# Kernel tuning notes

Measured on AMD Instinct MI355X. Metric: run time of the kernel, lower is better.

The kernel has to match this reference:

```python
import jax, jax.numpy as jnp
import numpy as np

B, S, D, H, T = 128, 256, 256, 1024, 128  # batch, src_len, input/output_dim, hidden, target_len


def setup_inputs() -> dict:
    key = jax.random.key(0)
    ks = jax.random.split(key, 16)
    sc = 0.05

    def p(k, shape):
        return (jax.random.normal(k, shape, jnp.float32) * sc)

    return {
        "x": jax.random.normal(ks[0], (B, S, D), jnp.float32),
        "x_target": jax.random.normal(ks[1], (B, T, D), jnp.float32),
        # encoder bidirectional LSTM (1 layer): gates order i,f,g,o (PyTorch)
        "enc_Wih_f": p(ks[2], (4 * H, D)),  "enc_Whh_f": p(ks[3], (4 * H, H)), "enc_b_f": p(ks[4], (4 * H,)),
        "enc_Wih_b": p(ks[5], (4 * H, D)),  "enc_Whh_b": p(ks[6], (4 * H, H)), "enc_b_b": p(ks[7], (4 * H,)),
        # decoder bidirectional LSTM (1 layer)
        "dec_Wih_f": p(ks[8], (4 * H, D)),  "dec_Whh_f": p(ks[9], (4 * H, H)), "dec_b_f": p(ks[10], (4 * H,)),
        "dec_Wih_b": p(ks[11], (4 * H, D)), "dec_Whh_b": p(ks[12], (4 * H, H)), "dec_b_b": p(ks[13], (4 * H,)),
        # decoder head: Linear(2H -> D)
        "mlp_W": p(ks[14], (D, 2 * H)), "mlp_b": p(ks[15], (D,)),
    }


def lstm_cell(x, h, c, Wih, Whh, b):
    # x: [B, Din], h/c: [B, H]; PyTorch gate order i, f, g, o
    g = x @ Wih.T + h @ Whh.T + b
    i, f, gg, o = jnp.split(g, 4, axis=-1)
    c = jax.nn.sigmoid(f) * c + jax.nn.sigmoid(i) * jnp.tanh(gg)
    h = jax.nn.sigmoid(o) * jnp.tanh(c)
    return h, c


def run_dir(xs, Wih, Whh, b, reverse):
    # xs: [S, B, Din]; returns final (h, c) for one direction (zero init, like torch LSTM without h0)
    h0 = jnp.zeros((xs.shape[1], Whh.shape[1]), xs.dtype)
    c0 = jnp.zeros_like(h0)

    def step(carry, xt):
        h, c = lstm_cell(xt, *carry, Wih, Whh, b)
        return (h, c), None

    (h, c), _ = jax.lax.scan(step, (h0, c0), xs, reverse=reverse)
    return h, c


def reference(x, x_target, enc_Wih_f, enc_Whh_f, enc_b_f, enc_Wih_b, enc_Whh_b, enc_b_b,
              dec_Wih_f, dec_Whh_f, dec_b_f, dec_Wih_b, dec_Whh_b, dec_b_b, mlp_W, mlp_b):
    xs = jnp.transpose(x, (1, 0, 2))  # [S, B, D], time-major
    hf, cf = run_dir(xs, enc_Wih_f, enc_Whh_f, enc_b_f, reverse=False)
    hb, cb = run_dir(xs, enc_Wih_b, enc_Whh_b, enc_b_b, reverse=True)

    dec_in = x[:, -1, :]  # [B, D]

    def step(carry, _):
        hf, cf, hb, cb, inp = carry
        # bidirectional LSTM on a length-1 sequence: both directions see the same step
        hf2, cf2 = lstm_cell(inp, hf, cf, dec_Wih_f, dec_Whh_f, dec_b_f)
        hb2, cb2 = lstm_cell(inp, hb, cb, dec_Wih_b, dec_Whh_b, dec_b_b)
        out = jnp.concatenate([hf2, hb2], axis=-1) @ mlp_W.T + mlp_b  # [B, D]
        # teacher_forcing_ratio = 0.0 -> always feed model output back
        return (hf2, cf2, hb2, cb2, out), out

    _, outs = jax.lax.scan(step, (hf, cf, hb, cb, dec_in), None, length=T)
    return jnp.transpose(outs, (1, 0, 2))  # [B, T, D]
```

## Files before the change

kernel.cpp:

```cpp
#include <hip/hip_runtime.h>
#include <stdint.h>


typedef __attribute__((ext_vector_type(8))) short bfx8;
typedef __attribute__((ext_vector_type(4))) float f32x4;
typedef __attribute__((ext_vector_type(4))) unsigned short u16x4;
typedef unsigned short ushort_t;
typedef unsigned long long u64;

#define NWG 256
#define MFMA(a,b,c) __builtin_amdgcn_mfma_f32_16x16x32_bf16((a),(b),(c),0,0,0)
#define WAITVM(N) { asm volatile("s_waitcnt vmcnt(" #N ")" ::: "memory"); __builtin_amdgcn_sched_barrier(0); }
#define WAITLG(N) { asm volatile("s_waitcnt lgkmcnt(" #N ")" ::: "memory"); __builtin_amdgcn_sched_barrier(0); }
#define SBAR()    { __builtin_amdgcn_s_barrier(); __builtin_amdgcn_sched_barrier(0); }

__device__ __forceinline__ unsigned short f2bf(float f){
  unsigned u = __float_as_uint(f);
  u += 0x7FFFu + ((u >> 16) & 1u);
  return (unsigned short)(u >> 16);
}
__device__ __forceinline__ float bf2f(unsigned short h){
  return __uint_as_float(((unsigned)h) << 16);
}
__device__ __forceinline__ float sigm(float x){ return 1.f/(1.f + __expf(-x)); }
__device__ __forceinline__ float tanh_(float x){ return 1.f - 2.f/(__expf(2.f*x) + 1.f); }

__device__ __forceinline__ void stage16(const void* g, void* l){
  __builtin_amdgcn_global_load_lds((const __attribute__((address_space(1))) void*)g,
                                   (__attribute__((address_space(3))) void*)l,
                                   16, 0, 0);
}
__device__ __forceinline__ void stage16c(const void* g, void* l){
  __builtin_amdgcn_global_load_lds((const __attribute__((address_space(1))) void*)g,
                                   (__attribute__((address_space(3))) void*)l,
                                   16, 0, 0x11);
}

__device__ __forceinline__ bfx8 ld16c(const ushort_t* p){
  const u64* q = (const u64*)p;
  u64 a = __hip_atomic_load(q,     __ATOMIC_RELAXED, __HIP_MEMORY_SCOPE_AGENT);
  u64 b = __hip_atomic_load(q + 1, __ATOMIC_RELAXED, __HIP_MEMORY_SCOPE_AGENT);
  union { u64 u[2]; bfx8 v; } x; x.u[0] = a; x.u[1] = b; return x.v;
}
__device__ __forceinline__ void sth2(ushort_t* p, unsigned short v){
  __hip_atomic_store(p, v, __ATOMIC_RELAXED, __HIP_MEMORY_SCOPE_AGENT);
}

__device__ __forceinline__ void cvt2(const f32x4& a, const f32x4& b, bfx8& hi, bfx8& lo){
#pragma unroll
  for (int j = 0; j < 4; ++j){
    unsigned short h0 = f2bf(a[j]);
    unsigned short h1 = f2bf(b[j]);
    hi[j]   = (short)h0; lo[j]   = (short)f2bf(a[j] - bf2f(h0));
    hi[4+j] = (short)h1; lo[4+j] = (short)f2bf(b[j] - bf2f(h1));
  }
}

__device__ __forceinline__ void bar(unsigned* flags, int nflags, int me, unsigned gen){
  __syncthreads();
  if (threadIdx.x == 0)
    __hip_atomic_store(&flags[me], gen, __ATOMIC_RELAXED, __HIP_MEMORY_SCOPE_AGENT);
  if (threadIdx.x < 64){
    const int l = threadIdx.x;
    for (;;){
      unsigned mn = 0xFFFFFFFFu;
      for (int o = l; o < nflags; o += 64){
        unsigned v = __hip_atomic_load(&flags[o], __ATOMIC_RELAXED, __HIP_MEMORY_SCOPE_AGENT);
        mn = mn < v ? mn : v;
      }
      if (__all((int)(mn >= gen))) break;
      __builtin_amdgcn_s_sleep(1);
    }
  }
  __syncthreads();
}

struct Frags { bfx8 awh0, awh1, awl0, awl1, bh0, bh1, bl0, bl1; };

template<int ENC>
__device__ __forceinline__ void cell_step(
    const float*    __restrict__ Wih,
    const ushort_t* __restrict__ WhH,
    const ushort_t* __restrict__ WhL,
    const float*    __restrict__ bias,
    const float*    __restrict__ xsl,
    const ushort_t* __restrict__ iph,
    const ushort_t* __restrict__ ipl,
    const ushort_t* __restrict__ hh,
    const ushort_t* __restrict__ hl,
    ushort_t* __restrict__ outh, ushort_t* __restrict__ outl,
    float (&creg)[2][2],
    int r0, int n0, int b0, ushort_t* LDS)
{
  const int tid  = threadIdx.x;
  const int lane = tid & 63;
  const int wv   = tid >> 6;
  const int wm   = wv >> 1, wn = wv & 1;
  const int lr   = tid >> 3;
  const int lc   = tid & 7;
  const int cb   = lane >> 4;
  const int fr   = lane & 15;
  const int sc8  = lc ^ (lr & 7);
  const int sx   = fr & 7;
  const int rwa0 = wm*32 + fr, rwa1 = rwa0 + 16;
  const int rwb0 = wn*32 + fr, rwb1 = rwb0 + 16;

  const int ra = r0 + lr, rb = ra + 32;
  const float* wih0 = Wih + (size_t)((ra & 3)*1024 + (ra >> 2))*256 + sc8*8;
  const float* wih1 = Wih + (size_t)((rb & 3)*1024 + (rb >> 2))*256 + sc8*8;
  const float *xs0 = nullptr, *xs1 = nullptr;
  const ushort_t *ih0 = nullptr, *ih1 = nullptr, *il0 = nullptr, *il1 = nullptr;
  if (ENC){
    xs0 = xsl + (size_t)(b0 + lr)*65536 + sc8*8;
    xs1 = xs0 + (size_t)32*65536;
  } else {
    ih0 = iph + (size_t)(b0 + lr)*256 + sc8*8;  ih1 = ih0 + 32*256;
    il0 = ipl + (size_t)(b0 + lr)*256 + sc8*8;  il1 = il0 + 32*256;
  }

  const ushort_t* sb; size_t sstr; int srow0;
  if      (wv == 0){ sb = WhH; sstr = 1024; srow0 = r0; }
  else if (wv == 1){ sb = WhL; sstr = 1024; srow0 = r0; }
  else if (wv == 2){ sb = hh;  sstr = 2048; srow0 = b0; }
  else             { sb = hl;  sstr = 2048; srow0 = b0; }
  const int srw = lane >> 3;
  const int sg  = (lane & 7) ^ srw;
  const ushort_t* pj[8];
#pragma unroll
  for (int j = 0; j < 8; ++j)
    pj[j] = sb + (size_t)(srow0 + j*8 + srw)*sstr + sg*8;
  ushort_t* ldsb[3];
#pragma unroll
  for (int bp = 0; bp < 3; ++bp)
    ldsb[bp] = LDS + 16384 + bp*16384 + wv*4096;

  auto ISSUE = [&](int c, int bp){
    const int ko = (c - 4)*64;
    if (wv < 2){
#pragma unroll
      for (int j = 0; j < 8; ++j)
        stage16(pj[j] + ko, ldsb[bp] + j*512);
    } else {
#pragma unroll
      for (int j = 0; j < 8; ++j)
        stage16c(pj[j] + ko, ldsb[bp] + j*512);
    }
  };

  f32x4 acc[2][2] = {};
  auto rdf = [&](const ushort_t* buf, int ks, Frags& f){
    const int ga = (((ks << 2) + cb) ^ sx) << 3;
    f.awh0 = *(const bfx8*)(buf +         rwa0*64 + ga);
    f.awh1 = *(const bfx8*)(buf +         rwa1*64 + ga);
    f.awl0 = *(const bfx8*)(buf + 4096  + rwa0*64 + ga);
    f.awl1 = *(const bfx8*)(buf + 4096  + rwa1*64 + ga);
    f.bh0  = *(const bfx8*)(buf + 8192  + rwb0*64 + ga);
    f.bh1  = *(const bfx8*)(buf + 8192  + rwb1*64 + ga);
    f.bl0  = *(const bfx8*)(buf + 12288 + rwb0*64 + ga);
    f.bl1  = *(const bfx8*)(buf + 12288 + rwb1*64 + ga);
  };
  auto mm12 = [&](const Frags& f){
    acc[0][0] = MFMA(f.awh0, f.bh0, acc[0][0]);
    acc[0][0] = MFMA(f.awh0, f.bl0, acc[0][0]);
    acc[0][0] = MFMA(f.awl0, f.bh0, acc[0][0]);
    acc[0][1] = MFMA(f.awh0, f.bh1, acc[0][1]);
    acc[0][1] = MFMA(f.awh0, f.bl1, acc[0][1]);
    acc[0][1] = MFMA(f.awl0, f.bh1, acc[0][1]);
    acc[1][0] = MFMA(f.awh1, f.bh0, acc[1][0]);
    acc[1][0] = MFMA(f.awh1, f.bl0, acc[1][0]);
    acc[1][0] = MFMA(f.awl1, f.bh0, acc[1][0]);
    acc[1][1] = MFMA(f.awh1, f.bh1, acc[1][1]);
    acc[1][1] = MFMA(f.awh1, f.bl1, acc[1][1]);
    acc[1][1] = MFMA(f.awl1, f.bh1, acc[1][1]);
  };

  f32x4 rw0a, rw0b, rw1a, rw1b, rxa0, rxb0, rxa1, rxb1;
  bfx8 cwh0, cwh1, cwl0, cwl1, cah0, cah1, cal0, cal1;
  auto LOADRAW = [&](int kc){
    rw0a = *(const f32x4*)(wih0 + kc);  rw0b = *(const f32x4*)(wih0 + kc + 4);
    rw1a = *(const f32x4*)(wih1 + kc);  rw1b = *(const f32x4*)(wih1 + kc + 4);
    if (ENC){
      rxa0 = *(const f32x4*)(xs0 + kc); rxb0 = *(const f32x4*)(xs0 + kc + 4);
      rxa1 = *(const f32x4*)(xs1 + kc); rxb1 = *(const f32x4*)(xs1 + kc + 4);
    } else {
      cah0 = ld16c(ih0 + kc);  cah1 = ld16c(ih1 + kc);
      cal0 = ld16c(il0 + kc);  cal1 = ld16c(il1 + kc);
    }
  };
  auto CVT = [&](){
    cvt2(rw0a, rw0b, cwh0, cwl0);
    cvt2(rw1a, rw1b, cwh1, cwl1);
    if (ENC){ cvt2(rxa0, rxb0, cah0, cal0); cvt2(rxa1, rxb1, cah1, cal1); }
  };

  LOADRAW(0);
  ISSUE(4, 0); ISSUE(5, 1); ISSUE(6, 2);
  CVT();

  for (int c = 0; c < 4; ++c){
    *(bfx8*)(LDS +         lr    *64 + lc*8) = cwh0;
    *(bfx8*)(LDS +        (lr+32)*64 + lc*8) = cwh1;
    *(bfx8*)(LDS + 4096 +  lr    *64 + lc*8) = cwl0;
    *(bfx8*)(LDS + 4096 + (lr+32)*64 + lc*8) = cwl1;
    *(bfx8*)(LDS + 8192 +  lr    *64 + lc*8) = cah0;
    *(bfx8*)(LDS + 8192 + (lr+32)*64 + lc*8) = cah1;
    *(bfx8*)(LDS + 12288 + lr    *64 + lc*8) = cal0;
    *(bfx8*)(LDS + 12288 +(lr+32)*64 + lc*8) = cal1;
    WAITLG(0); SBAR();
    if (c < 3) LOADRAW((c + 1)*64);
    Frags f0, f1;
    rdf(LDS, 0, f0);
    rdf(LDS, 1, f1);
    WAITLG(8);
    mm12(f0);
    WAITLG(0); SBAR();
    if (c < 3) CVT();
    mm12(f1);
  }

  int bi = 0;
  for (int i = 4; i <= 19; ++i){
    if (i < 18)      { WAITVM(16); }
    else if (i == 18){ WAITVM(8); }
    else             { WAITVM(0); }
    SBAR();
    const ushort_t* buf = LDS + 16384 + bi*16384;
    Frags f0, f1;
    rdf(buf, 0, f0);
    rdf(buf, 1, f1);
    WAITLG(8);
    mm12(f0);
    WAITLG(0); SBAR();
    if (i <= 16) ISSUE(i + 3, bi);
    mm12(f1);
    bi = (bi == 2) ? 0 : bi + 1;
  }

#pragma unroll
  for (int m = 0; m < 2; ++m){
    const int n = n0 + wm*8 + m*4 + cb;
    const float bi_ = bias[n];
    const float bf_ = bias[1024 + n];
    const float bg_ = bias[2048 + n];
    const float bo_ = bias[3072 + n];
#pragma unroll
    for (int nb = 0; nb < 2; ++nb){
      const int b = b0 + wn*32 + nb*16 + fr;
      float gi = acc[m][nb][0] + bi_;
      float gf = acc[m][nb][1] + bf_;
      float gg = acc[m][nb][2] + bg_;
      float go = acc[m][nb][3] + bo_;
      float c_new = sigm(gf)*creg[m][nb] + sigm(gi)*tanh_(gg);
      float h_new = sigm(go)*tanh_(c_new);
      creg[m][nb] = c_new;
      unsigned short hi = f2bf(h_new);
      sth2(&outh[(size_t)b*2048 + n], hi);
      sth2(&outl[(size_t)b*2048 + n], f2bf(h_new - bf2f(hi)));
    }
  }
}

__device__ __forceinline__ void mlp_gemm(
    const ushort_t* __restrict__ hch, const ushort_t* __restrict__ hcl,
    const ushort_t* __restrict__ mWh, const ushort_t* __restrict__ mWl,
    float* __restrict__ Part, int wg, ushort_t* LDS)
{
  const int tid = threadIdx.x, lane = tid & 63, wv = tid >> 6;
  const int cb = lane >> 4, fr = lane & 15, sx = fr & 7;
  const int wgl = wg & 127, kh = wg >> 7;
  const int d0 = (wgl >> 3)*16, b0 = (wgl & 7)*16;
  const int kb = kh*1024 + wv*256;
  const int srw = lane >> 3, sg = (lane & 7) ^ srw;

  const ushort_t* ps[4] = { mWh, mWl, hch, hcl };
  const int pr0[4] = { d0, d0, b0, b0 };
  const ushort_t* pj[4][2];
#pragma unroll
  for (int p = 0; p < 4; ++p)
#pragma unroll
    for (int j = 0; j < 2; ++j)
      pj[p][j] = ps[p] + (size_t)(pr0[p] + j*8 + srw)*2048 + kb + sg*8;
  ushort_t* lb[3];
#pragma unroll
  for (int bp = 0; bp < 3; ++bp)
    lb[bp] = LDS + 16384 + (wv*3 + bp)*4096;

  auto ISSUE = [&](int c, int bp){
    const int ko = c*64;
#pragma unroll
    for (int p = 0; p < 4; ++p)
#pragma unroll
      for (int j = 0; j < 2; ++j){
        if (p < 2) stage16 (pj[p][j] + ko, lb[bp] + p*1024 + j*512);
        else       stage16c(pj[p][j] + ko, lb[bp] + p*1024 + j*512);
      }
  };
  ISSUE(0, 0); ISSUE(1, 1); ISSUE(2, 2);

  f32x4 acc = {};
  int bp = 0;
  for (int c = 0; c < 4; ++c){
    if (c < 2)      { WAITVM(16); }
    else if (c == 2){ WAITVM(8); }
    else            { WAITVM(0); }
    const ushort_t* B = lb[bp];
    const int ga0 = ((cb) ^ sx) << 3;
    const int ga1 = ((4 + cb) ^ sx) << 3;
    bfx8 wh0 = *(const bfx8*)(B +        fr*64 + ga0);
    bfx8 wl0 = *(const bfx8*)(B + 1024 + fr*64 + ga0);
    bfx8 ah0 = *(const bfx8*)(B + 2048 + fr*64 + ga0);
    bfx8 al0 = *(const bfx8*)(B + 3072 + fr*64 + ga0);
    bfx8 wh1 = *(const bfx8*)(B +        fr*64 + ga1);
    bfx8 wl1 = *(const bfx8*)(B + 1024 + fr*64 + ga1);
    bfx8 ah1 = *(const bfx8*)(B + 2048 + fr*64 + ga1);
    bfx8 al1 = *(const bfx8*)(B + 3072 + fr*64 + ga1);
    WAITLG(0);
    if (c == 0) ISSUE(3, 0);
    acc = MFMA(wh0, ah0, acc); acc = MFMA(wh0, al0, acc); acc = MFMA(wl0, ah0, acc);
    acc = MFMA(wh1, ah1, acc); acc = MFMA(wh1, al1, acc); acc = MFMA(wl1, ah1, acc);
    bp = (bp == 2) ? 0 : bp + 1;
  }
  u64* P8 = (u64*)Part;
  const size_t idx = (((size_t)wgl*2 + kh)*4 + wv)*64 + lane;
  u64 a = ((u64)__float_as_uint(acc[1]) << 32) | __float_as_uint(acc[0]);
  u64 b = ((u64)__float_as_uint(acc[3]) << 32) | __float_as_uint(acc[2]);
  __hip_atomic_store(&P8[2*idx],     a, __ATOMIC_RELAXED, __HIP_MEMORY_SCOPE_AGENT);
  __hip_atomic_store(&P8[2*idx + 1], b, __ATOMIC_RELAXED, __HIP_MEMORY_SCOPE_AGENT);
}

__device__ __forceinline__ void mlp_combine(
    const float* __restrict__ Part, const float* __restrict__ mb,
    float* __restrict__ dout,
    ushort_t* __restrict__ inph, ushort_t* __restrict__ inpl, int wg, int t)
{
  if (threadIdx.x >= 64) return;
  const int lane = threadIdx.x;
  const int d0 = (wg >> 3)*16, b0 = (wg & 7)*16;
  const int cb = lane >> 4, fr = lane & 15;
  const u64* P8 = (const u64*)Part;
  f32x4 s = {};
#pragma unroll
  for (int kh = 0; kh < 2; ++kh)
#pragma unroll
    for (int wv = 0; wv < 4; ++wv){
      const size_t idx = (((size_t)wg*2 + kh)*4 + wv)*64 + lane;
      u64 a = __hip_atomic_load(&P8[2*idx],     __ATOMIC_RELAXED, __HIP_MEMORY_SCOPE_AGENT);
      u64 b = __hip_atomic_load(&P8[2*idx + 1], __ATOMIC_RELAXED, __HIP_MEMORY_SCOPE_AGENT);
      s[0] += __uint_as_float((unsigned)a);
      s[1] += __uint_as_float((unsigned)(a >> 32));
      s[2] += __uint_as_float((unsigned)b);
      s[3] += __uint_as_float((unsigned)(b >> 32));
    }
  const int dr = d0 + cb*4, b = b0 + fr;
  s += *(const f32x4*)&mb[dr];
  *(f32x4*)&dout[((size_t)b*128 + t)*256 + dr] = s;
  u16x4 hv, lv;
#pragma unroll
  for (int j = 0; j < 4; ++j){
    hv[j] = f2bf(s[j]);
    lv[j] = f2bf(s[j] - bf2f(hv[j]));
  }
  union { u16x4 v; u64 u; } ch, cl; ch.v = hv; cl.v = lv;
  __hip_atomic_store((u64*)&inph[(size_t)b*256 + dr], ch.u, __ATOMIC_RELAXED, __HIP_MEMORY_SCOPE_AGENT);
  __hip_atomic_store((u64*)&inpl[(size_t)b*256 + dr], cl.u, __ATOMIC_RELAXED, __HIP_MEMORY_SCOPE_AGENT);
}

__device__ __forceinline__ void wg_decode(int wg, int& dir, int& r0, int& n0,
                                          int& b0, int& me){
  const int half = (wg >> 3) & 1;
  const int rgd  = (wg & 7) | ((wg >> 4) << 3);
  dir = rgd >> 6;
  const int rg = rgd & 63;
  r0 = rg * 64; n0 = rg * 16; b0 = half * 64;
  me = (rg << 1) | half;
}

__global__ void __launch_bounds__(256) rnn_enc_kernel(
    const float* __restrict__ Wih_f, const float* __restrict__ b_f,
    const float* __restrict__ Wih_b, const float* __restrict__ b_b,
    const ushort_t* __restrict__ WhhH, const ushort_t* __restrict__ WhhL,
    const float* __restrict__ x,
    ushort_t* __restrict__ Hh, ushort_t* __restrict__ Hl,
    float* __restrict__ C, unsigned* flagsE)
{
  extern __shared__ ushort_t LDS[];
  int dir, r0, n0, b0, me;
  wg_decode(blockIdx.x, dir, r0, n0, b0, me);
  const float* Wih = dir ? Wih_b : Wih_f;
  const float* bia = dir ? b_b : b_f;
  const ushort_t* WhH = WhhH + (size_t)dir*4096*1024;
  const ushort_t* WhL = WhhL + (size_t)dir*4096*1024;
  unsigned* fl = flagsE + dir*128;
  float creg[2][2] = {{0.f, 0.f}, {0.f, 0.f}};
  unsigned gen = 0;
  for (int t = 0; t < 256; ++t){
    const int tt = dir ? (255 - t) : t;
    const int rp = t & 1;
    cell_step<1>(Wih, WhH, WhL, bia,
                 x + (size_t)tt*256, nullptr, nullptr,
                 Hh + (size_t)rp     *262144 + dir*1024,
                 Hl + (size_t)rp     *262144 + dir*1024,
                 Hh + (size_t)(rp^1) *262144 + dir*1024,
                 Hl + (size_t)(rp^1) *262144 + dir*1024,
                 creg, r0, n0, b0, LDS);
    ++gen;
    bar(fl, 128, me, gen);
  }
  {
    const int lane = threadIdx.x & 63, wv = threadIdx.x >> 6;
    const int wm = wv >> 1, wn = wv & 1, cb = lane >> 4, fr = lane & 15;
    float* Cst = C + (size_t)dir*1024*128;
#pragma unroll
    for (int m = 0; m < 2; ++m)
#pragma unroll
      for (int nb = 0; nb < 2; ++nb){
        const int n = n0 + wm*8 + m*4 + cb;
        const int b = b0 + wn*32 + nb*16 + fr;
        Cst[n*128 + b] = creg[m][nb];
      }
  }
}

__global__ void __launch_bounds__(256) rnn_dec_kernel(
    const float* __restrict__ Wih_f, const float* __restrict__ b_f,
    const float* __restrict__ Wih_b, const float* __restrict__ b_b,
    const ushort_t* __restrict__ WhhH, const ushort_t* __restrict__ WhhL,
    const ushort_t* __restrict__ mWh, const ushort_t* __restrict__ mWl,
    const float* __restrict__ mb,
    ushort_t* __restrict__ Hh, ushort_t* __restrict__ Hl,
    float* __restrict__ C,
    ushort_t* __restrict__ inph, ushort_t* __restrict__ inpl,
    float* __restrict__ Part,
    float* __restrict__ dout, unsigned* flagsD)
{
  extern __shared__ ushort_t LDS[];
  const int wg = blockIdx.x;
  int dir, r0, n0, b0, me;
  wg_decode(wg, dir, r0, n0, b0, me);
  const float* Wih = dir ? Wih_b : Wih_f;
  const float* bia = dir ? b_b : b_f;
  const ushort_t* WhH = WhhH + (size_t)dir*4096*1024;
  const ushort_t* WhL = WhhL + (size_t)dir*4096*1024;
  float creg[2][2];
  {
    const int lane = threadIdx.x & 63, wv = threadIdx.x >> 6;
    const int wm = wv >> 1, wn = wv & 1, cb = lane >> 4, fr = lane & 15;
    const float* Cst = C + (size_t)dir*1024*128;
#pragma unroll
    for (int m = 0; m < 2; ++m)
#pragma unroll
      for (int nb = 0; nb < 2; ++nb){
        const int n = n0 + wm*8 + m*4 + cb;
        const int b = b0 + wn*32 + nb*16 + fr;
        creg[m][nb] = Cst[n*128 + b];
      }
  }
  for (int t = 0; t < 128; ++t){
    const int rp = t & 1;
    cell_step<0>(Wih, WhH, WhL, bia,
                 nullptr, inph, inpl,
                 Hh + (size_t)rp     *262144 + dir*1024,
                 Hl + (size_t)rp     *262144 + dir*1024,
                 Hh + (size_t)(rp^1) *262144 + dir*1024,
                 Hl + (size_t)(rp^1) *262144 + dir*1024,
                 creg, r0, n0, b0, LDS);
    bar(flagsD, 256, wg, (unsigned)(3*t + 1));
    mlp_gemm(Hh + (size_t)(rp^1)*262144, Hl + (size_t)(rp^1)*262144,
             mWh, mWl, Part, wg, LDS);
    bar(flagsD, 256, wg, (unsigned)(3*t + 2));
    if (wg < 128) mlp_combine(Part, mb, dout, inph, inpl, wg, t);
    bar(flagsD, 256, wg, (unsigned)(3*t + 3));
  }
}

__global__ void k_wplanes(ushort_t* Hp, ushort_t* Lp,
                          const float* Whh_f, const float* Whh_b)
{
  const size_t N = 2ull*4096*1024;
  for (size_t i = (size_t)blockIdx.x*blockDim.x + threadIdx.x; i < N;
       i += (size_t)gridDim.x*blockDim.x){
    int dir = (int)(i >> 22);
    int r   = (int)((i >> 10) & 4095);
    int k   = (int)(i & 1023);
    int n = r >> 2, q = r & 3;
    const float* W = dir ? Whh_b : Whh_f;
    float v = W[(size_t)(q*1024 + n)*1024 + k];
    unsigned short h = f2bf(v);
    Hp[i] = h;
    Lp[i] = f2bf(v - bf2f(h));
  }
}

__global__ void k_init(ushort_t* Hh, ushort_t* Hl,
                       ushort_t* inph, ushort_t* inpl,
                       ushort_t* mWh, ushort_t* mWl,
                       const float* x, const float* mW, unsigned* cnt)
{
  const size_t N = 524288;
  for (size_t i = (size_t)blockIdx.x*blockDim.x + threadIdx.x; i < N;
       i += (size_t)gridDim.x*blockDim.x){
    Hh[i] = 0; Hl[i] = 0;
    float wv = mW[i];
    unsigned short wh = f2bf(wv);
    mWh[i] = wh;
    mWl[i] = f2bf(wv - bf2f(wh));
    if (i < 32768){
      int b = (int)(i >> 8), d = (int)(i & 255);
      float v = x[((size_t)b*256 + 255)*256 + d];
      unsigned short hi = f2bf(v);
      inph[i] = hi;
      inpl[i] = f2bf(v - bf2f(hi));
    }
    if (i < 1024) cnt[i] = 0;
  }
}

extern "C" void kernel_launch(void* const* d_in, const int* in_sizes, int n_in,
                              void* d_out, int out_size, void* d_ws, size_t ws_size,
                              hipStream_t stream)
{
  (void)in_sizes; (void)n_in; (void)out_size; (void)ws_size;
  const float* x      = (const float*)d_in[0];
  const float* eWih_f = (const float*)d_in[2];
  const float* eWhh_f = (const float*)d_in[3];
  const float* eb_f   = (const float*)d_in[4];
  const float* eWih_b = (const float*)d_in[5];
  const float* eWhh_b = (const float*)d_in[6];
  const float* eb_b   = (const float*)d_in[7];
  const float* dWih_f = (const float*)d_in[8];
  const float* dWhh_f = (const float*)d_in[9];
  const float* db_f   = (const float*)d_in[10];
  const float* dWih_b = (const float*)d_in[11];
  const float* dWhh_b = (const float*)d_in[12];
  const float* db_b   = (const float*)d_in[13];
  const float* mW     = (const float*)d_in[14];
  const float* mb     = (const float*)d_in[15];

  char* p = (char*)d_ws;
  size_t off = 0;
  unsigned* cnt   = (unsigned*)(p + off);  off += 4096;
  ushort_t* WhhEh = (ushort_t*)(p + off);  off += 16777216;
  ushort_t* WhhEl = (ushort_t*)(p + off);  off += 16777216;
  ushort_t* WhhDh = (ushort_t*)(p + off);  off += 16777216;
  ushort_t* WhhDl = (ushort_t*)(p + off);  off += 16777216;
  ushort_t* mWh   = (ushort_t*)(p + off);  off += 1048576;
  ushort_t* mWl   = (ushort_t*)(p + off);  off += 1048576;
  ushort_t* Hh    = (ushort_t*)(p + off);  off += 1048576;
  ushort_t* Hl    = (ushort_t*)(p + off);  off += 1048576;
  float*    C     = (float*)(p + off);     off += 1048576;
  ushort_t* inph  = (ushort_t*)(p + off);  off += 65536;
  ushort_t* inpl  = (ushort_t*)(p + off);  off += 65536;
  float*    Part  = (float*)(p + off);     off += 1048576;

  unsigned* flagsD = cnt;
  unsigned* flagsE = cnt + 256;

  hipFuncSetAttribute(reinterpret_cast<const void*>(rnn_enc_kernel),
                      hipFuncAttributeMaxDynamicSharedMemorySize, 131072);
  hipFuncSetAttribute(reinterpret_cast<const void*>(rnn_dec_kernel),
                      hipFuncAttributeMaxDynamicSharedMemorySize, 131072);

  k_init   <<<512, 256, 0, stream>>>(Hh, Hl, inph, inpl, mWh, mWl, x, mW, cnt);
  k_wplanes<<<2048, 256, 0, stream>>>(WhhEh, WhhEl, eWhh_f, eWhh_b);
  k_wplanes<<<2048, 256, 0, stream>>>(WhhDh, WhhDl, dWhh_f, dWhh_b);

  rnn_enc_kernel<<<NWG, 256, 131072, stream>>>(eWih_f, eb_f, eWih_b, eb_b,
                                               WhhEh, WhhEl, x, Hh, Hl, C, flagsE);
  rnn_dec_kernel<<<NWG, 256, 131072, stream>>>(dWih_f, db_f, dWih_b, db_b,
                                               WhhDh, WhhDl, mWh, mWl, mb,
                                               Hh, Hl, C, inph, inpl, Part,
                                               (float*)d_out, flagsD);
}
```

Before: 10.12 ms.

## Prefetch encoder recurrent weights during grid barrier and deepen h staging pipeline

Splits the encoder cell into its own function that issues all four input-projection chunk loads up front. It then streams the recurrent weight planes through a two-slot ring and the hidden-state planes through a separate five-slot ring. A new barrier variant issues the first two weight chunks for the next timestep before spinning on the grid flags, so the weight fetch overlaps the inter-workgroup sync. This hides global load latency on the serial recurrence path, at the cost of more LDS (dynamic shared memory raised) and more registers, with hand-tuned vmcnt waits that must match the issue order exactly.

```diff
diff --git a/kernel.cpp b/kernel.cpp
--- a/kernel.cpp
+++ b/kernel.cpp
@@ -13,6 +13,7 @@
 #define WAITVM(N) { asm volatile("s_waitcnt vmcnt(" #N ")" ::: "memory"); __builtin_amdgcn_sched_barrier(0); }
 #define WAITLG(N) { asm volatile("s_waitcnt lgkmcnt(" #N ")" ::: "memory"); __builtin_amdgcn_sched_barrier(0); }
 #define SBAR()    { __builtin_amdgcn_s_barrier(); __builtin_amdgcn_sched_barrier(0); }
+#define SCHED0()  __builtin_amdgcn_sched_barrier(0)
 
 __device__ __forceinline__ unsigned short f2bf(float f){
   unsigned u = __float_as_uint(f);
@@ -75,19 +76,49 @@
   __syncthreads();
 }
 
+struct WPre {
+  const ushort_t* pj[8];
+  ushort_t* ldsb[2];
+  bool active;
+};
+__device__ __forceinline__ void wpre_issue(const WPre& w){
+  if (!w.active) return;
+#pragma unroll
+  for (int bp = 0; bp < 2; ++bp)
+#pragma unroll
+    for (int j = 0; j < 8; ++j)
+      stage16(w.pj[j] + bp*64, w.ldsb[bp] + j*512);
+}
+__device__ __forceinline__ void bar_pf(unsigned* flags, int nflags, int me,
+                                       unsigned gen, const WPre& w, bool pf){
+  WAITLG(0); WAITVM(0);
+  SBAR();
+  if (pf) wpre_issue(w);
+  if (threadIdx.x == 192)
+    __hip_atomic_store(&flags[me], gen, __ATOMIC_RELAXED, __HIP_MEMORY_SCOPE_AGENT);
+  if ((threadIdx.x >> 6) == 3){
+    const int l = threadIdx.x & 63;
+    for (;;){
+      unsigned mn = 0xFFFFFFFFu;
+      for (int o = l; o < nflags; o += 64){
+        unsigned v = __hip_atomic_load(&flags[o], __ATOMIC_RELAXED, __HIP_MEMORY_SCOPE_AGENT);
+        mn = mn < v ? mn : v;
+      }
+      if (__all((int)(mn >= gen))) break;
+      __builtin_amdgcn_s_sleep(1);
+    }
+  }
+  SBAR();
+}
+
 struct Frags { bfx8 awh0, awh1, awl0, awl1, bh0, bh1, bl0, bl1; };
 
-template<int ENC>
-__device__ __forceinline__ void cell_step(
+__device__ __forceinline__ void cell_enc(
     const float*    __restrict__ Wih,
-    const ushort_t* __restrict__ WhH,
-    const ushort_t* __restrict__ WhL,
+    const ushort_t* __restrict__ WhH, const ushort_t* __restrict__ WhL,
     const float*    __restrict__ bias,
     const float*    __restrict__ xsl,
-    const ushort_t* __restrict__ iph,
-    const ushort_t* __restrict__ ipl,
-    const ushort_t* __restrict__ hh,
-    const ushort_t* __restrict__ hl,
+    const ushort_t* __restrict__ hh, const ushort_t* __restrict__ hl,
     ushort_t* __restrict__ outh, ushort_t* __restrict__ outl,
     float (&creg)[2][2],
     int r0, int n0, int b0, ushort_t* LDS)
@@ -108,15 +139,8 @@
   const int ra = r0 + lr, rb = ra + 32;
   const float* wih0 = Wih + (size_t)((ra & 3)*1024 + (ra >> 2))*256 + sc8*8;
   const float* wih1 = Wih + (size_t)((rb & 3)*1024 + (rb >> 2))*256 + sc8*8;
-  const float *xs0 = nullptr, *xs1 = nullptr;
-  const ushort_t *ih0 = nullptr, *ih1 = nullptr, *il0 = nullptr, *il1 = nullptr;
-  if (ENC){
-    xs0 = xsl + (size_t)(b0 + lr)*65536 + sc8*8;
-    xs1 = xs0 + (size_t)32*65536;
-  } else {
-    ih0 = iph + (size_t)(b0 + lr)*256 + sc8*8;  ih1 = ih0 + 32*256;
-    il0 = ipl + (size_t)(b0 + lr)*256 + sc8*8;  il1 = il0 + 32*256;
-  }
+  const float* xs0 = xsl + (size_t)(b0 + lr)*65536 + sc8*8;
+  const float* xs1 = xs0 + (size_t)32*65536;
 
   const ushort_t* sb; size_t sstr; int srow0;
   if      (wv == 0){ sb = WhH; sstr = 1024; srow0 = r0; }
@@ -129,35 +153,42 @@
 #pragma unroll
   for (int j = 0; j < 8; ++j)
     pj[j] = sb + (size_t)(srow0 + j*8 + srw)*sstr + sg*8;
-  ushort_t* ldsb[3];
-#pragma unroll
-  for (int bp = 0; bp < 3; ++bp)
-    ldsb[bp] = LDS + 16384 + bp*16384 + wv*4096;
-
-  auto ISSUE = [&](int c, int bp){
+
+  auto ISSUE_W = [&](int c, int s){
     const int ko = (c - 4)*64;
-    if (wv < 2){
-#pragma unroll
-      for (int j = 0; j < 8; ++j)
-        stage16(pj[j] + ko, ldsb[bp] + j*512);
-    } else {
-#pragma unroll
-      for (int j = 0; j < 8; ++j)
-        stage16c(pj[j] + ko, ldsb[bp] + j*512);
-    }
+    ushort_t* d = LDS + 16384 + s*8192 + (wv & 1)*4096;
+#pragma unroll
+    for (int j = 0; j < 8; ++j) stage16(pj[j] + ko, d + j*512);
+  };
+  auto ISSUE_H = [&](int c, int s){
+    const int ko = (c - 4)*64;
+    ushort_t* d = LDS + 32768 + s*8192 + (wv & 1)*4096;
+#pragma unroll
+    for (int j = 0; j < 8; ++j) stage16c(pj[j] + ko, d + j*512);
   };
 
   f32x4 acc[2][2] = {};
-  auto rdf = [&](const ushort_t* buf, int ks, Frags& f){
+  auto rdf = [&](const ushort_t* wb, const ushort_t* ab, int ks, Frags& f){
     const int ga = (((ks << 2) + cb) ^ sx) << 3;
-    f.awh0 = *(const bfx8*)(buf +         rwa0*64 + ga);
-    f.awh1 = *(const bfx8*)(buf +         rwa1*64 + ga);
-    f.awl0 = *(const bfx8*)(buf + 4096  + rwa0*64 + ga);
-    f.awl1 = *(const bfx8*)(buf + 4096  + rwa1*64 + ga);
-    f.bh0  = *(const bfx8*)(buf + 8192  + rwb0*64 + ga);
-    f.bh1  = *(const bfx8*)(buf + 8192  + rwb1*64 + ga);
-    f.bl0  = *(const bfx8*)(buf + 12288 + rwb0*64 + ga);
-    f.bl1  = *(const bfx8*)(buf + 12288 + rwb1*64 + ga);
+    f.awh0 = *(const bfx8*)(wb +        rwa0*64 + ga);
+    f.awh1 = *(const bfx8*)(wb +        rwa1*64 + ga);
+    f.awl0 = *(const bfx8*)(wb + 4096 + rwa0*64 + ga);
+    f.awl1 = *(const bfx8*)(wb + 4096 + rwa1*64 + ga);
+    f.bh0  = *(const bfx8*)(ab +        rwb0*64 + ga);
+    f.bh1  = *(const bfx8*)(ab +        rwb1*64 + ga);
+    f.bl0  = *(const bfx8*)(ab + 2048 + rwb0*64 + ga);
+    f.bl1  = *(const bfx8*)(ab + 2048 + rwb1*64 + ga);
+  };
+  auto rdf3 = [&](const ushort_t* wb, const ushort_t* ab, int ks, Frags& f){
+    const int ga = (((ks << 2) + cb) ^ sx) << 3;
+    f.awh0 = *(const bfx8*)(wb +        rwa0*64 + ga);
+    f.awh1 = *(const bfx8*)(wb +        rwa1*64 + ga);
+    f.awl0 = *(const bfx8*)(wb + 4096 + rwa0*64 + ga);
+    f.awl1 = *(const bfx8*)(wb + 4096 + rwa1*64 + ga);
+    f.bh0  = *(const bfx8*)(ab +        rwb0*64 + ga);
+    f.bh1  = *(const bfx8*)(ab +        rwb1*64 + ga);
+    f.bl0  = *(const bfx8*)(ab + 4096 + rwb0*64 + ga);
+    f.bl1  = *(const bfx8*)(ab + 4096 + rwb1*64 + ga);
   };
   auto mm12 = [&](const Frags& f){
     acc[0][0] = MFMA(f.awh0, f.bh0, acc[0][0]);
@@ -173,24 +204,231 @@
     acc[1][1] = MFMA(f.awh1, f.bl1, acc[1][1]);
     acc[1][1] = MFMA(f.awl1, f.bh1, acc[1][1]);
   };
-
-  f32x4 rw0a, rw0b, rw1a, rw1b, rxa0, rxb0, rxa1, rxb1;
+  (void)rdf3;
+
+  f32x4 rw[4][4], rx[4][4];
+#pragma unroll
+  for (int c = 0; c < 4; ++c){
+    const int kc = c*64;
+    rw[c][0] = *(const f32x4*)(wih0 + kc);  rw[c][1] = *(const f32x4*)(wih0 + kc + 4);
+    rw[c][2] = *(const f32x4*)(wih1 + kc);  rw[c][3] = *(const f32x4*)(wih1 + kc + 4);
+    rx[c][0] = *(const f32x4*)(xs0 + kc);   rx[c][1] = *(const f32x4*)(xs0 + kc + 4);
+    rx[c][2] = *(const f32x4*)(xs1 + kc);   rx[c][3] = *(const f32x4*)(xs1 + kc + 4);
+  }
+  SCHED0();
+  if (wv >= 2){
+#pragma unroll
+    for (int s = 0; s < 5; ++s) ISSUE_H(4 + s, s);
+  }
+  SCHED0();
+  bfx8 swh[4][2], swl[4][2], sah[4][2], sal[4][2];
+#pragma unroll
+  for (int c = 0; c < 4; ++c){
+    cvt2(rw[c][0], rw[c][1], swh[c][0], swl[c][0]);
+    cvt2(rw[c][2], rw[c][3], swh[c][1], swl[c][1]);
+    cvt2(rx[c][0], rx[c][1], sah[c][0], sal[c][0]);
+    cvt2(rx[c][2], rx[c][3], sah[c][1], sal[c][1]);
+  }
+
+#pragma unroll
+  for (int c = 0; c < 4; ++c){
+    *(bfx8*)(LDS +         lr    *64 + lc*8) = swh[c][0];
+    *(bfx8*)(LDS +        (lr+32)*64 + lc*8) = swh[c][1];
+    *(bfx8*)(LDS + 4096 +  lr    *64 + lc*8) = swl[c][0];
+    *(bfx8*)(LDS + 4096 + (lr+32)*64 + lc*8) = swl[c][1];
+    *(bfx8*)(LDS + 8192 +  lr    *64 + lc*8) = sah[c][0];
+    *(bfx8*)(LDS + 8192 + (lr+32)*64 + lc*8) = sah[c][1];
+    *(bfx8*)(LDS + 12288 + lr    *64 + lc*8) = sal[c][0];
+    *(bfx8*)(LDS + 12288 +(lr+32)*64 + lc*8) = sal[c][1];
+    WAITLG(0); SBAR();
+    Frags f0, f1;
+    { const int ga0 = ((cb) ^ sx) << 3, ga1 = ((4 + cb) ^ sx) << 3;
+      f0.awh0 = *(const bfx8*)(LDS +        rwa0*64 + ga0);
+      f0.awh1 = *(const bfx8*)(LDS +        rwa1*64 + ga0);
+      f0.awl0 = *(const bfx8*)(LDS + 4096 + rwa0*64 + ga0);
+      f0.awl1 = *(const bfx8*)(LDS + 4096 + rwa1*64 + ga0);
+      f0.bh0  = *(const bfx8*)(LDS + 8192 + rwb0*64 + ga0);
+      f0.bh1  = *(const bfx8*)(LDS + 8192 + rwb1*64 + ga0);
+      f0.bl0  = *(const bfx8*)(LDS + 12288+ rwb0*64 + ga0);
+      f0.bl1  = *(const bfx8*)(LDS + 12288+ rwb1*64 + ga0);
+      f1.awh0 = *(const bfx8*)(LDS +        rwa0*64 + ga1);
+      f1.awh1 = *(const bfx8*)(LDS +        rwa1*64 + ga1);
+      f1.awl0 = *(const bfx8*)(LDS + 4096 + rwa0*64 + ga1);
+      f1.awl1 = *(const bfx8*)(LDS + 4096 + rwa1*64 + ga1);
+      f1.bh0  = *(const bfx8*)(LDS + 8192 + rwb0*64 + ga1);
+      f1.bh1  = *(const bfx8*)(LDS + 8192 + rwb1*64 + ga1);
+      f1.bl0  = *(const bfx8*)(LDS + 12288+ rwb0*64 + ga1);
+      f1.bl1  = *(const bfx8*)(LDS + 12288+ rwb1*64 + ga1);
+    }
+    WAITLG(8);
+    mm12(f0);
+    WAITLG(0); SBAR();
+    mm12(f1);
+  }
+
+  int hcs = 0, his = 0;
+  for (int i = 4; i <= 19; ++i){
+    if (wv < 2){
+      if (i <= 18) { WAITVM(8); } else { WAITVM(0); }
+    } else {
+      if      (i <= 15) { WAITVM(32); }
+      else if (i == 16) { WAITVM(24); }
+      else if (i == 17) { WAITVM(16); }
+      else if (i == 18) { WAITVM(8); }
+      else              { WAITVM(0); }
+    }
+    SBAR();
+    const ushort_t* wb = LDS + 16384 + (i & 1)*8192;
+    const ushort_t* ab = LDS + 32768 + hcs*8192;
+    Frags f0, f1;
+    { const int ga0 = ((cb) ^ sx) << 3, ga1 = ((4 + cb) ^ sx) << 3;
+      f0.awh0 = *(const bfx8*)(wb +        rwa0*64 + ga0);
+      f0.awh1 = *(const bfx8*)(wb +        rwa1*64 + ga0);
+      f0.awl0 = *(const bfx8*)(wb + 4096 + rwa0*64 + ga0);
+      f0.awl1 = *(const bfx8*)(wb + 4096 + rwa1*64 + ga0);
+      f0.bh0  = *(const bfx8*)(ab +        rwb0*64 + ga0);
+      f0.bh1  = *(const bfx8*)(ab +        rwb1*64 + ga0);
+      f0.bl0  = *(const bfx8*)(ab + 4096 + rwb0*64 + ga0);
+      f0.bl1  = *(const bfx8*)(ab + 4096 + rwb1*64 + ga0);
+      f1.awh0 = *(const bfx8*)(wb +        rwa0*64 + ga1);
+      f1.awh1 = *(const bfx8*)(wb +        rwa1*64 + ga1);
+      f1.awl0 = *(const bfx8*)(wb + 4096 + rwa0*64 + ga1);
+      f1.awl1 = *(const bfx8*)(wb + 4096 + rwa1*64 + ga1);
+      f1.bh0  = *(const bfx8*)(ab +        rwb0*64 + ga1);
+      f1.bh1  = *(const bfx8*)(ab +        rwb1*64 + ga1);
+      f1.bl0  = *(const bfx8*)(ab + 4096 + rwb0*64 + ga1);
+      f1.bl1  = *(const bfx8*)(ab + 4096 + rwb1*64 + ga1);
+    }
+    WAITLG(8);
+    mm12(f0);
+    WAITLG(0); SBAR();
+    if (wv < 2){ if (i <= 17) ISSUE_W(i + 2, i & 1); }
+    else       { if (i <= 14) ISSUE_H(i + 5, his); }
+    mm12(f1);
+    hcs = (hcs == 4) ? 0 : hcs + 1;
+    his = (his == 4) ? 0 : his + 1;
+  }
+
+#pragma unroll
+  for (int m = 0; m < 2; ++m){
+    const int n = n0 + wm*8 + m*4 + cb;
+    const float bi_ = bias[n];
+    const float bf_ = bias[1024 + n];
+    const float bg_ = bias[2048 + n];
+    const float bo_ = bias[3072 + n];
+#pragma unroll
+    for (int nb = 0; nb < 2; ++nb){
+      const int b = b0 + wn*32 + nb*16 + fr;
+      float gi = acc[m][nb][0] + bi_;
+      float gf = acc[m][nb][1] + bf_;
+      float gg = acc[m][nb][2] + bg_;
+      float go = acc[m][nb][3] + bo_;
+      float c_new = sigm(gf)*creg[m][nb] + sigm(gi)*tanh_(gg);
+      float h_new = sigm(go)*tanh_(c_new);
+      creg[m][nb] = c_new;
+      unsigned short hi = f2bf(h_new);
+      sth2(&outh[(size_t)b*2048 + n], hi);
+      sth2(&outl[(size_t)b*2048 + n], f2bf(h_new - bf2f(hi)));
+    }
+  }
+}
+
+__device__ __forceinline__ void cell_dec(
+    const float*    __restrict__ Wih,
+    const ushort_t* __restrict__ WhH, const ushort_t* __restrict__ WhL,
+    const float*    __restrict__ bias,
+    const ushort_t* __restrict__ iph, const ushort_t* __restrict__ ipl,
+    const ushort_t* __restrict__ hh,  const ushort_t* __restrict__ hl,
+    ushort_t* __restrict__ outh, ushort_t* __restrict__ outl,
+    float (&creg)[2][2],
+    int r0, int n0, int b0, ushort_t* LDS)
+{
+  const int tid  = threadIdx.x;
+  const int lane = tid & 63;
+  const int wv   = tid >> 6;
+  const int wm   = wv >> 1, wn = wv & 1;
+  const int lr   = tid >> 3;
+  const int lc   = tid & 7;
+  const int cb   = lane >> 4;
+  const int fr   = lane & 15;
+  const int sc8  = lc ^ (lr & 7);
+  const int sx   = fr & 7;
+  const int rwa0 = wm*32 + fr, rwa1 = rwa0 + 16;
+  const int rwb0 = wn*32 + fr, rwb1 = rwb0 + 16;
+
+  const int ra = r0 + lr, rb = ra + 32;
+  const float* wih0 = Wih + (size_t)((ra & 3)*1024 + (ra >> 2))*256 + sc8*8;
+  const float* wih1 = Wih + (size_t)((rb & 3)*1024 + (rb >> 2))*256 + sc8*8;
+  const ushort_t* ih0 = iph + (size_t)(b0 + lr)*256 + sc8*8;
+  const ushort_t* ih1 = ih0 + 32*256;
+  const ushort_t* il0 = ipl + (size_t)(b0 + lr)*256 + sc8*8;
+  const ushort_t* il1 = il0 + 32*256;
+
+  const ushort_t* sb; size_t sstr; int srow0;
+  if      (wv == 0){ sb = WhH; sstr = 1024; srow0 = r0; }
+  else if (wv == 1){ sb = WhL; sstr = 1024; srow0 = r0; }
+  else if (wv == 2){ sb = hh;  sstr = 2048; srow0 = b0; }
+  else             { sb = hl;  sstr = 2048; srow0 = b0; }
+  const int srw = lane >> 3;
+  const int sg  = (lane & 7) ^ srw;
+  const ushort_t* pj[8];
+#pragma unroll
+  for (int j = 0; j < 8; ++j)
+    pj[j] = sb + (size_t)(srow0 + j*8 + srw)*sstr + sg*8;
+  ushort_t* ldsb[3];
+#pragma unroll
+  for (int bp = 0; bp < 3; ++bp)
+    ldsb[bp] = LDS + 16384 + bp*16384 + wv*4096;
+
+  auto ISSUE = [&](int c, int bp){
+    const int ko = (c - 4)*64;
+    if (wv < 2){
+#pragma unroll
+      for (int j = 0; j < 8; ++j) stage16(pj[j] + ko, ldsb[bp] + j*512);
+    } else {
+#pragma unroll
+      for (int j = 0; j < 8; ++j) stage16c(pj[j] + ko, ldsb[bp] + j*512);
+    }
+  };
+
+  f32x4 acc[2][2] = {};
+  auto rdf = [&](const ushort_t* buf, int ks, Frags& f){
+    const int ga = (((ks << 2) + cb) ^ sx) << 3;
+    f.awh0 = *(const bfx8*)(buf +         rwa0*64 + ga);
+    f.awh1 = *(const bfx8*)(buf +         rwa1*64 + ga);
+    f.awl0 = *(const bfx8*)(buf + 4096  + rwa0*64 + ga);
+    f.awl1 = *(const bfx8*)(buf + 4096  + rwa1*64 + ga);
+    f.bh0  = *(const bfx8*)(buf + 8192  + rwb0*64 + ga);
+    f.bh1  = *(const bfx8*)(buf + 8192  + rwb1*64 + ga);
+    f.bl0  = *(const bfx8*)(buf + 12288 + rwb0*64 + ga);
+    f.bl1  = *(const bfx8*)(buf + 12288 + rwb1*64 + ga);
+  };
+  auto mm12 = [&](const Frags& f){
+    acc[0][0] = MFMA(f.awh0, f.bh0, acc[0][0]);
+    acc[0][0] = MFMA(f.awh0, f.bl0, acc[0][0]);
+    acc[0][0] = MFMA(f.awl0, f.bh0, acc[0][0]);
+    acc[0][1] = MFMA(f.awh0, f.bh1, acc[0][1]);
+    acc[0][1] = MFMA(f.awh0, f.bl1, acc[0][1]);
+    acc[0][1] = MFMA(f.awl0, f.bh1, acc[0][1]);
+    acc[1][0] = MFMA(f.awh1, f.bh0, acc[1][0]);
+    acc[1][0] = MFMA(f.awh1, f.bl0, acc[1][0]);
+    acc[1][0] = MFMA(f.awl1, f.bh0, acc[1][0]);
+    acc[1][1] = MFMA(f.awh1, f.bh1, acc[1][1]);
+    acc[1][1] = MFMA(f.awh1, f.bl1, acc[1][1]);
+    acc[1][1] = MFMA(f.awl1, f.bh1, acc[1][1]);
+  };
+
+  f32x4 rw0a, rw0b, rw1a, rw1b;
   bfx8 cwh0, cwh1, cwl0, cwl1, cah0, cah1, cal0, cal1;
   auto LOADRAW = [&](int kc){
     rw0a = *(const f32x4*)(wih0 + kc);  rw0b = *(const f32x4*)(wih0 + kc + 4);
     rw1a = *(const f32x4*)(wih1 + kc);  rw1b = *(const f32x4*)(wih1 + kc + 4);
-    if (ENC){
-      rxa0 = *(const f32x4*)(xs0 + kc); rxb0 = *(const f32x4*)(xs0 + kc + 4);
-      rxa1 = *(const f32x4*)(xs1 + kc); rxb1 = *(const f32x4*)(xs1 + kc + 4);
-    } else {
-      cah0 = ld16c(ih0 + kc);  cah1 = ld16c(ih1 + kc);
-      cal0 = ld16c(il0 + kc);  cal1 = ld16c(il1 + kc);
-    }
+    cah0 = ld16c(ih0 + kc);  cah1 = ld16c(ih1 + kc);
+    cal0 = ld16c(il0 + kc);  cal1 = ld16c(il1 + kc);
   };
   auto CVT = [&](){
     cvt2(rw0a, rw0b, cwh0, cwl0);
     cvt2(rw1a, rw1b, cwh1, cwl1);
-    if (ENC){ cvt2(rxa0, rxb0, cah0, cal0); cvt2(rxa1, rxb1, cah1, cal1); }
   };
 
   LOADRAW(0);
@@ -375,6 +613,23 @@
   me = (rg << 1) | half;
 }
 
+__device__ __forceinline__ WPre make_wpre(const ushort_t* WhH, const ushort_t* WhL,
+                                          int r0, ushort_t* LDS){
+  const int tid = threadIdx.x, lane = tid & 63, wv = tid >> 6;
+  const int srw = lane >> 3;
+  const int sg  = (lane & 7) ^ srw;
+  WPre w;
+  w.active = (wv < 2);
+  const ushort_t* sb = (wv == 1) ? WhL : WhH;
+#pragma unroll
+  for (int j = 0; j < 8; ++j)
+    w.pj[j] = sb + (size_t)(r0 + j*8 + srw)*1024 + sg*8;
+#pragma unroll
+  for (int s = 0; s < 2; ++s)
+    w.ldsb[s] = LDS + 16384 + s*8192 + (wv & 1)*4096;
+  return w;
+}
+
 __global__ void __launch_bounds__(256) rnn_enc_kernel(
     const float* __restrict__ Wih_f, const float* __restrict__ b_f,
     const float* __restrict__ Wih_b, const float* __restrict__ b_b,
@@ -391,20 +646,21 @@
   const ushort_t* WhH = WhhH + (size_t)dir*4096*1024;
   const ushort_t* WhL = WhhL + (size_t)dir*4096*1024;
   unsigned* fl = flagsE + dir*128;
+  const WPre wp = make_wpre(WhH, WhL, r0, LDS);
+
   float creg[2][2] = {{0.f, 0.f}, {0.f, 0.f}};
-  unsigned gen = 0;
+  wpre_issue(wp);
   for (int t = 0; t < 256; ++t){
     const int tt = dir ? (255 - t) : t;
     const int rp = t & 1;
-    cell_step<1>(Wih, WhH, WhL, bia,
-                 x + (size_t)tt*256, nullptr, nullptr,
-                 Hh + (size_t)rp     *262144 + dir*1024,
-                 Hl + (size_t)rp     *262144 + dir*1024,
-                 Hh + (size_t)(rp^1) *262144 + dir*1024,
-                 Hl + (size_t)(rp^1) *262144 + dir*1024,
-                 creg, r0, n0, b0, LDS);
-    ++gen;
-    bar(fl, 128, me, gen);
+    cell_enc(Wih, WhH, WhL, bia,
+             x + (size_t)tt*256,
+             Hh + (size_t)rp     *262144 + dir*1024,
+             Hl + (size_t)rp     *262144 + dir*1024,
+             Hh + (size_t)(rp^1) *262144 + dir*1024,
+             Hl + (size_t)(rp^1) *262144 + dir*1024,
+             creg, r0, n0, b0, LDS);
+    bar_pf(fl, 128, me, (unsigned)(t + 1), wp, t < 255);
   }
   {
     const int lane = threadIdx.x & 63, wv = threadIdx.x >> 6;
@@ -457,13 +713,13 @@
   }
   for (int t = 0; t < 128; ++t){
     const int rp = t & 1;
-    cell_step<0>(Wih, WhH, WhL, bia,
-                 nullptr, inph, inpl,
-                 Hh + (size_t)rp     *262144 + dir*1024,
-                 Hl + (size_t)rp     *262144 + dir*1024,
-                 Hh + (size_t)(rp^1) *262144 + dir*1024,
-                 Hl + (size_t)(rp^1) *262144 + dir*1024,
-                 creg, r0, n0, b0, LDS);
+    cell_dec(Wih, WhH, WhL, bia,
+             inph, inpl,
+             Hh + (size_t)rp     *262144 + dir*1024,
+             Hl + (size_t)rp     *262144 + dir*1024,
+             Hh + (size_t)(rp^1) *262144 + dir*1024,
+             Hl + (size_t)(rp^1) *262144 + dir*1024,
+             creg, r0, n0, b0, LDS);
     bar(flagsD, 256, wg, (unsigned)(3*t + 1));
     mlp_gemm(Hh + (size_t)(rp^1)*262144, Hl + (size_t)(rp^1)*262144,
              mWh, mWl, Part, wg, LDS);
@@ -511,7 +767,7 @@
       inph[i] = hi;
       inpl[i] = f2bf(v - bf2f(hi));
     }
-    if (i < 1024) cnt[i] = 0;
+    if (i < 2048) cnt[i] = 0;
   }
 }
 
@@ -538,7 +794,7 @@
 
   char* p = (char*)d_ws;
   size_t off = 0;
-  unsigned* cnt   = (unsigned*)(p + off);  off += 4096;
+  unsigned* cnt   = (unsigned*)(p + off);  off += 8192;
   ushort_t* WhhEh = (ushort_t*)(p + off);  off += 16777216;
   ushort_t* WhhEl = (ushort_t*)(p + off);  off += 16777216;
   ushort_t* WhhDh = (ushort_t*)(p + off);  off += 16777216;
@@ -556,7 +812,7 @@
   unsigned* flagsE = cnt + 256;
 
   hipFuncSetAttribute(reinterpret_cast<const void*>(rnn_enc_kernel),
-                      hipFuncAttributeMaxDynamicSharedMemorySize, 131072);
+                      hipFuncAttributeMaxDynamicSharedMemorySize, 147456);
   hipFuncSetAttribute(reinterpret_cast<const void*>(rnn_dec_kernel),
                       hipFuncAttributeMaxDynamicSharedMemorySize, 131072);
 
@@ -564,7 +820,7 @@
   k_wplanes<<<2048, 256, 0, stream>>>(WhhEh, WhhEl, eWhh_f, eWhh_b);
   k_wplanes<<<2048, 256, 0, stream>>>(WhhDh, WhhDl, dWhh_f, dWhh_b);
 
-  rnn_enc_kernel<<<NWG, 256, 131072, stream>>>(eWih_f, eb_f, eWih_b, eb_b,
+  rnn_enc_kernel<<<NWG, 256, 147456, stream>>>(eWih_f, eb_f, eWih_b, eb_b,
                                                WhhEh, WhhEl, x, Hh, Hl, C, flagsE);
   rnn_dec_kernel<<<NWG, 256, 131072, stream>>>(dWih_f, db_f, dWih_b, db_b,
                                                WhhDh, WhhDl, mWh, mWl, mb,
```

Result: faster. 9.900 ms (-2.2%).
